# Kernel optimization log

Measured on AMD Instinct MI355X. Metric: run time of the kernel, lower is better.

## Reference

```python
import jax, jax.numpy as jnp
import numpy as np

# dims: B batch, T frames, N tokens/frame, C embed, H heads, D=C//H, MEM memory slots
B, T, N, C = 8, 16, 196, 768
H = 8
D = C // H
MEM = 196          # mem_size; with N=196 -> _init_t = 1, M stays == MEM
HID = 4 * C        # mlp_ratio * embed_dim
STD = 0.02


def _mlp(x, w1, b1, w2, b2):
    # timm-style Mlp: fc1 -> GELU -> fc2 (dropout = 0)
    return jax.nn.gelu(x @ w1 + b1, approximate=False) @ w2 + b2


def _ln(x, w, b, eps=1e-5):
    mu = jnp.mean(x, axis=-1, keepdims=True)
    var = jnp.var(x, axis=-1, keepdims=True)
    return (x - mu) * jax.lax.rsqrt(var + eps) * w + b


def setup_inputs() -> dict:
    key = jax.random.key(0)
    ks = jax.random.split(key, 10)
    f32 = jnp.float32
    return {
        "cur_fea": jax.random.normal(ks[0], (B, T, N, C), f32),
        "norm1_w": jnp.ones((C,), f32), "norm1_b": jnp.zeros((C,), f32),
        "norm2_w": jnp.ones((C,), f32), "norm2_b": jnp.zeros((C,), f32),
        # c_func: Mlp(2C -> 4C -> C)
        "c_w1": jax.random.normal(ks[1], (2 * C, HID), f32) * STD, "c_b1": jnp.zeros((HID,), f32),
        "c_w2": jax.random.normal(ks[2], (HID, C), f32) * STD, "c_b2": jnp.zeros((C,), f32),
        # m_func: Mlp(C -> 4C -> C)
        "m_w1": jax.random.normal(ks[3], (C, HID), f32) * STD, "m_b1": jnp.zeros((HID,), f32),
        "m_w2": jax.random.normal(ks[4], (HID, C), f32) * STD, "m_b2": jnp.zeros((C,), f32),
        # post_func: Mlp(C -> 4C -> C)
        "p_w1": jax.random.normal(ks[5], (C, HID), f32) * STD, "p_b1": jnp.zeros((HID,), f32),
        "p_w2": jax.random.normal(ks[6], (HID, C), f32) * STD, "p_b2": jnp.zeros((C,), f32),
        # ProjectDotDistance: per-head q(c_global) . k(mem) * scale -> sigmoid
        "q_w": jax.random.normal(ks[7], (C, C), f32) * STD, "q_b": jnp.zeros((C,), f32),
        "k_w": jax.random.normal(ks[8], (C, C), f32) * STD, "k_b": jnp.zeros((C,), f32),
    }


def reference(cur_fea, norm1_w, norm1_b, norm2_w, norm2_b,
              c_w1, c_b1, c_w2, c_b2, m_w1, m_b1, m_w2, m_b2,
              p_w1, p_b1, p_w2, p_b2, q_w, q_b, k_w, k_b):
    x = _ln(cur_fea, norm1_w, norm1_b)                       # [B,T,N,C]
    # T*N > mem_size, _init_t = MEM // N = 1 -> init memory = frame 0 (no grad, torch.no_grad)
    init_mem = jax.lax.stop_gradient(x[:, 0].reshape(B, MEM, C))
    scale = D ** -0.5

    def step(mem, fea):                                      # mem [B,MEM,C], fea [B,N,C]
        ap = jnp.mean(mem, axis=1, keepdims=True)            # [B,1,C]
        cg = _mlp(jnp.concatenate([fea, jnp.broadcast_to(ap, fea.shape)], axis=-1),
                  c_w1, c_b1, c_w2, c_b2)                    # [B,N,C]
        memh = _mlp(mem, m_w1, m_b1, m_w2, m_b2).reshape(B, MEM, H, D).transpose(0, 2, 1, 3)  # [B,H,M,D]
        q = (cg @ q_w + q_b).reshape(B, N, H, D).transpose(0, 2, 1, 3)    # [B,H,N,D]
        k = (mem @ k_w + k_b).reshape(B, MEM, H, D).transpose(0, 2, 1, 3) # [B,H,M,D]
        o = jax.nn.sigmoid(jnp.einsum('bhnd,bhmd->bhnm', q, k) * scale)   # [B,H,N,M]
        cgh = cg.reshape(B, N, H, D).transpose(0, 2, 1, 3)               # [B,H,N,D]
        c = jnp.einsum('bhnm,bhnd->bmhd', o, cgh).reshape(B, MEM, C)
        c = _mlp(c, p_w1, p_b1, p_w2, p_b2)
        # mean_N((1-o) * broadcast(memh)) == mean_N(1-o) * memh (memh indep of N)
        gate = jnp.mean(1.0 - o, axis=2)                     # [B,H,M]
        og = (gate[..., None] * memh).transpose(0, 2, 1, 3).reshape(B, MEM, C)
        new_mem = _ln(c + og, norm2_w, norm2_b)
        return new_mem, None

    fea_seq = x[:, 1:].transpose(1, 0, 2, 3)                 # [T-1,B,N,C]
    final_mem, _ = jax.lax.scan(step, init_mem, fea_seq)
    return final_mem                                         # [B,MEM,C]
```

## Files before the change

kernel.cpp:

```cpp
#include <hip/hip_runtime.h>
#include <hip/hip_bf16.h>
#include <math.h>

constexpr int B_   = 8;
constexpr int T_   = 16;
constexpr int N_   = 196;
constexpr int C_   = 768;
constexpr int H_   = 8;
constexpr int D_   = 96;
constexpr int M_   = 196;
constexpr int HID_ = 3072;
constexpr int ROWS_ = B_ * N_;
constexpr int MP_   = 1664;

typedef __hip_bfloat16 bf16;
typedef __attribute__((ext_vector_type(8))) short bf16x8;
typedef __attribute__((ext_vector_type(4))) float f32x4;

__device__ __forceinline__ float b2f(bf16 x) { return __bfloat162float(x); }
__device__ __forceinline__ short bf2s(bf16 x) { union { bf16 b; short s; } u; u.b = x; return u.s; }
__device__ __forceinline__ float s2f(short x) { union { bf16 b; short s; } u; u.s = x; return __bfloat162float(u.b); }

#define GL2LDS(g, l) __builtin_amdgcn_global_load_lds( \
    (__attribute__((address_space(1))) void*)(g), \
    (__attribute__((address_space(3))) void*)(l), 16, 0, 0)

__device__ __forceinline__ void hard_barrier() {
    asm volatile("" ::: "memory");
    __builtin_amdgcn_s_barrier();
    asm volatile("" ::: "memory");
}


__device__ __forceinline__ float block_reduce_sum256(float v, float* sdata) {
    int tid = threadIdx.x;
    sdata[tid] = v;
    __syncthreads();
    for (int s = 128; s > 0; s >>= 1) {
        if (tid < s) sdata[tid] += sdata[tid + s];
        __syncthreads();
    }
    float r = sdata[0];
    __syncthreads();
    return r;
}

struct TEnt { const float* W; bf16* Wt; int K; int N; int tiles; };
struct TEnts { TEnt e[8]; };

__global__ __launch_bounds__(256) void transpose_all_kernel(TEnts tds)
{
    __shared__ float tile[32][33];
    int local = blockIdx.x;
    int i = 0;
    while (i < 7 && local >= tds.e[i].tiles) { local -= tds.e[i].tiles; ++i; }
    TEnt g = tds.e[i];
    int ntx = g.N / 32;
    int n0 = (local % ntx) * 32, k0 = (local / ntx) * 32;
    int tx = threadIdx.x & 31, ty = threadIdx.x >> 5;
#pragma unroll
    for (int r = 0; r < 32; r += 8)
        tile[ty + r][tx] = g.W[(size_t)(k0 + ty + r) * g.N + n0 + tx];
    __syncthreads();
#pragma unroll
    for (int r = 0; r < 32; r += 8)
        g.Wt[(size_t)(n0 + ty + r) * g.K + k0 + tx] = __float2bfloat16(tile[tx][ty + r]);
}

__global__ __launch_bounds__(256) void cvt_kernel(const float* __restrict__ W,
                                                  bf16* __restrict__ o, int n)
{
    int i = blockIdx.x * 256 + threadIdx.x;
    if (i < n) o[i] = __float2bfloat16(W[i]);
}

__global__ __launch_bounds__(256) void ln_frame_kernel(
    const float* __restrict__ cur, int t,
    const float* __restrict__ w, const float* __restrict__ bia,
    bf16* __restrict__ mem_bf, float* __restrict__ app)
{
    __shared__ float sdata[256];
    int row = blockIdx.x;
    int b = row / N_, n = row % N_;
    const float* src = cur + (((size_t)b * T_ + t) * N_ + n) * C_;
    float x[3];
    float sum = 0.f, sumsq = 0.f;
#pragma unroll
    for (int i = 0; i < 3; i++) {
        int c = threadIdx.x + i * 256;
        x[i] = src[c];
        sum += x[i]; sumsq += x[i] * x[i];
    }
    sum = block_reduce_sum256(sum, sdata);
    sumsq = block_reduce_sum256(sumsq, sdata);
    float mu = sum * (1.0f / C_);
    float var = sumsq * (1.0f / C_) - mu * mu;
    float rs = rsqrtf(var + 1e-5f);
#pragma unroll
    for (int i = 0; i < 3; i++) {
        int c = threadIdx.x + i * 256;
        bf16 hv = __float2bfloat16((x[i] - mu) * rs * w[c] + bia[c]);
        mem_bf[(size_t)row * C_ + c] = hv;
        atomicAdd(&app[(size_t)b * C_ + c], b2f(hv));
    }
}

__global__ __launch_bounds__(256) void build_cat_kernel(
    const float* __restrict__ cur, int t,
    const float* __restrict__ w, const float* __restrict__ bia,
    const float* __restrict__ app, bf16* __restrict__ cat)
{
    __shared__ float sdata[256];
    int row = blockIdx.x;
    int b = row / N_, n = row % N_;
    const float* src = cur + (((size_t)b * T_ + t) * N_ + n) * C_;
    float x[3];
    float sum = 0.f, sumsq = 0.f;
#pragma unroll
    for (int i = 0; i < 3; i++) {
        int c = threadIdx.x + i * 256;
        x[i] = src[c];
        sum += x[i]; sumsq += x[i] * x[i];
    }
    sum = block_reduce_sum256(sum, sdata);
    sumsq = block_reduce_sum256(sumsq, sdata);
    float mu = sum * (1.0f / C_);
    float var = sumsq * (1.0f / C_) - mu * mu;
    float rs = rsqrtf(var + 1e-5f);
    bf16* dstrow = cat + (size_t)row * (2 * C_);
#pragma unroll
    for (int i = 0; i < 3; i++) {
        int c = threadIdx.x + i * 256;
        dstrow[c] = __float2bfloat16((x[i] - mu) * rs * w[c] + bia[c]);
        dstrow[C_ + c] = __float2bfloat16(app[(size_t)b * C_ + c] * (1.0f / M_));
    }
}

struct GemmDesc {
    const bf16* A; const bf16* W; const float* bias; bf16* out;
    int K; int N; int ymax; int gelu;
};
struct GemmDescs { GemmDesc d[4]; };

template <int BN>
__global__ __launch_bounds__(256) void mfma_gemm_multi(GemmDescs ds)
{
    constexpr int BM = 128;
    constexpr int TI = 4;
    constexpr int TJ = (BN / 2) / 16;
    constexpr int ABYTES = BM * 128;
    constexpr int BBYTES = BN * 128;
    constexpr int AR = ABYTES / 4096;
    constexpr int BR = BBYTES / 4096;
    constexpr int NL = AR + BR;
    __shared__ short As[2 * BM * 64];
    __shared__ short Bs[2 * BN * 64];

    GemmDesc g = ds.d[blockIdx.z];
    if ((int)blockIdx.y >= g.ymax) return;

    int tid = threadIdx.x;
    int wid = tid >> 6;
    int lane = tid & 63;
    int quad = lane >> 4, l15 = lane & 15;
    int row0 = blockIdx.x * BM;
    int col0 = blockIdx.y * BN;
    int wm = (wid >> 1) * 64;
    int wn = (wid & 1) * (BN / 2);

    f32x4 acc[TI][TJ] = {};

    const char* Ab = (const char*)g.A;
    const char* Wb = (const char*)g.W;
    const size_t Kb = (size_t)g.K * 2;
    const int base = wid * 1024;

    auto stage = [&](int k0, int sel) {
        char* Ad = (char*)As + sel * ABYTES;
        char* Bd = (char*)Bs + sel * BBYTES;
#pragma unroll
        for (int r = 0; r < AR; r++) {
            int o = r * 4096 + base + lane * 16;
            int row = o >> 7, cs = (o >> 4) & 7;
            int kc = cs ^ (row & 7);
            GL2LDS(Ab + (size_t)(row0 + row) * Kb + (size_t)k0 * 2 + kc * 16, Ad + o);
        }
#pragma unroll
        for (int r = 0; r < BR; r++) {
            int o = r * 4096 + base + lane * 16;
            int row = o >> 7, cs = (o >> 4) & 7;
            int kc = cs ^ (row & 7);
            GL2LDS(Wb + (size_t)(col0 + row) * Kb + (size_t)k0 * 2 + kc * 16, Bd + o);
        }
    };

    const int nk = g.K / 64;
    stage(0, 0);
    for (int ki = 0; ki < nk; ki++) {
        int sel = ki & 1;
        if (ki + 1 < nk) {
            stage((ki + 1) * 64, sel ^ 1);
            asm volatile("s_waitcnt vmcnt(%0)" :: "n"(NL) : "memory");
        } else {
            asm volatile("s_waitcnt vmcnt(0)" ::: "memory");
        }
        hard_barrier();
        const bf16x8* Av = (const bf16x8*)(As + sel * BM * 64);
        const bf16x8* Bv = (const bf16x8*)(Bs + sel * BN * 64);
        bf16x8 af[TI][2], bfr[TJ][2];
#pragma unroll
        for (int i = 0; i < TI; i++) {
            int r = wm + i * 16 + l15;
#pragma unroll
            for (int hh = 0; hh < 2; hh++)
                af[i][hh] = Av[r * 8 + ((hh * 4 + quad) ^ (r & 7))];
        }
#pragma unroll
        for (int j = 0; j < TJ; j++) {
            int r = wn + j * 16 + l15;
#pragma unroll
            for (int hh = 0; hh < 2; hh++)
                bfr[j][hh] = Bv[r * 8 + ((hh * 4 + quad) ^ (r & 7))];
        }
#pragma unroll
        for (int hh = 0; hh < 2; hh++)
#pragma unroll
            for (int i = 0; i < TI; i++)
#pragma unroll
                for (int j = 0; j < TJ; j++)
                    acc[i][j] = __builtin_amdgcn_mfma_f32_16x16x32_bf16(
                        af[i][hh], bfr[j][hh], acc[i][j], 0, 0, 0);
        hard_barrier();
    }

#pragma unroll
    for (int i = 0; i < TI; i++) {
        int gr = row0 + wm + i * 16 + quad * 4;
#pragma unroll
        for (int j = 0; j < TJ; j++) {
            int gc = col0 + wn + j * 16 + l15;
            float bv = g.bias ? g.bias[gc] : 0.0f;
#pragma unroll
            for (int r = 0; r < 4; r++) {
                float v = acc[i][j][r] + bv;
                if (g.gelu) v = 0.5f * v * (1.0f + erff(v * 0.7071067811865475f));
                g.out[(size_t)(gr + r) * g.N + gc] = __float2bfloat16(v);
            }
        }
    }
}

__global__ __launch_bounds__(256) void mfma_gemm_splitk(
    const bf16* __restrict__ A, const bf16* __restrict__ Wt,
    float* __restrict__ part, int K)
{
    constexpr int BM = 128;
    constexpr int BN = 64;
    constexpr int TI = 4;
    constexpr int TJ = 2;
    constexpr int ABYTES = BM * 128, BBYTES = BN * 128;
    constexpr int AR = 4, BR = 2, NL = 6;
    __shared__ short As[2 * BM * 64];
    __shared__ short Bs[2 * BN * 64];

    int tid = threadIdx.x;
    int wid = tid >> 6;
    int lane = tid & 63;
    int quad = lane >> 4, l15 = lane & 15;
    int row0 = blockIdx.x * BM;
    int col0 = blockIdx.y * BN;
    int wm = (wid >> 1) * 64;
    int wn = (wid & 1) * 32;
    int kh = K >> 1;
    int kbeg = blockIdx.z * kh;

    f32x4 acc[TI][TJ] = {};
    const char* Ab = (const char*)A;
    const char* Wb = (const char*)Wt;
    const size_t Kb = (size_t)K * 2;
    const int base = wid * 1024;

    auto stage = [&](int k0, int sel) {
        char* Ad = (char*)As + sel * ABYTES;
        char* Bd = (char*)Bs + sel * BBYTES;
#pragma unroll
        for (int r = 0; r < AR; r++) {
            int o = r * 4096 + base + lane * 16;
            int row = o >> 7, cs = (o >> 4) & 7;
            int kc = cs ^ (row & 7);
            GL2LDS(Ab + (size_t)(row0 + row) * Kb + (size_t)k0 * 2 + kc * 16, Ad + o);
        }
#pragma unroll
        for (int r = 0; r < BR; r++) {
            int o = r * 4096 + base + lane * 16;
            int row = o >> 7, cs = (o >> 4) & 7;
            int kc = cs ^ (row & 7);
            GL2LDS(Wb + (size_t)(col0 + row) * Kb + (size_t)k0 * 2 + kc * 16, Bd + o);
        }
    };

    const int nk = kh / 64;
    stage(kbeg, 0);
    for (int ki = 0; ki < nk; ki++) {
        int sel = ki & 1;
        if (ki + 1 < nk) {
            stage(kbeg + (ki + 1) * 64, sel ^ 1);
            asm volatile("s_waitcnt vmcnt(%0)" :: "n"(NL) : "memory");
        } else {
            asm volatile("s_waitcnt vmcnt(0)" ::: "memory");
        }
        hard_barrier();
        const bf16x8* Av = (const bf16x8*)(As + sel * BM * 64);
        const bf16x8* Bv = (const bf16x8*)(Bs + sel * BN * 64);
        bf16x8 af[TI][2], bfr[TJ][2];
#pragma unroll
        for (int i = 0; i < TI; i++) {
            int r = wm + i * 16 + l15;
#pragma unroll
            for (int hh = 0; hh < 2; hh++)
                af[i][hh] = Av[r * 8 + ((hh * 4 + quad) ^ (r & 7))];
        }
#pragma unroll
        for (int j = 0; j < TJ; j++) {
            int r = wn + j * 16 + l15;
#pragma unroll
            for (int hh = 0; hh < 2; hh++)
                bfr[j][hh] = Bv[r * 8 + ((hh * 4 + quad) ^ (r & 7))];
        }
#pragma unroll
        for (int hh = 0; hh < 2; hh++)
#pragma unroll
            for (int i = 0; i < TI; i++)
#pragma unroll
                for (int j = 0; j < TJ; j++)
                    acc[i][j] = __builtin_amdgcn_mfma_f32_16x16x32_bf16(
                        af[i][hh], bfr[j][hh], acc[i][j], 0, 0, 0);
        hard_barrier();
    }

    float* outp = part + (size_t)blockIdx.z * MP_ * C_;
#pragma unroll
    for (int i = 0; i < TI; i++) {
        int gr = row0 + wm + i * 16 + quad * 4;
#pragma unroll
        for (int j = 0; j < TJ; j++) {
            int gc = col0 + wn + j * 16 + l15;
#pragma unroll
            for (int r = 0; r < 4; r++)
                outp[(size_t)(gr + r) * C_ + gc] = acc[i][j][r];
        }
    }
}

__global__ __launch_bounds__(256) void b2q_kernel(
    const float* __restrict__ c_b2, const float* __restrict__ q_b,
    const bf16* __restrict__ W2q_t, float* __restrict__ b2q)
{
    __shared__ float sdata[256];
    int n = blockIdx.x;
    const bf16* row = W2q_t + (size_t)n * HID_;
    float s = 0.f;
    for (int j = threadIdx.x; j < HID_; j += 256) s += c_b2[j] * b2f(row[j]);
    s = block_reduce_sum256(s, sdata);
    if (threadIdx.x == 0) b2q[n] = s + q_b[n];
}

__global__ __launch_bounds__(512) void attn_mfma_kernel(
    const bf16* __restrict__ q, const bf16* __restrict__ k,
    const bf16* __restrict__ cg, bf16* __restrict__ cbuf,
    float* __restrict__ gate)
{
    constexpr int KS = 104;
    constexpr int PSS = 40;
    __shared__ short Ks[64 * KS];
    __shared__ short Qs[32 * KS];
    __shared__ short CGt[96 * PSS];
    __shared__ short Ph[64 * PSS];
    __shared__ short Pl[64 * PSS];
    __shared__ float gred[8][64];

    const int mt = blockIdx.x, h = blockIdx.y, b = blockIdx.z;
    const int m0 = (mt < 3) ? mt * 64 : (M_ - 64);
    const int tid = threadIdx.x;
    const int w = tid >> 6, lane = tid & 63;
    const int quad = lane >> 4, l15 = lane & 15;
    const int wm = w >> 1;
    const int wh = w & 1;
    const float scale = 0.10206207261596575f;

    const bf16* qp = q  + (size_t)b * N_ * C_ + h * D_;
    const bf16* kp = k  + (size_t)b * M_ * C_ + h * D_;
    const bf16* cp = cg + (size_t)b * N_ * C_ + h * D_;

    for (int idx = tid; idx < 64 * 12; idx += 512) {
        int r = idx / 12, c = idx % 12;
        *(bf16x8*)(Ks + r * KS + c * 8) =
            *(const bf16x8*)(kp + (size_t)(m0 + r) * C_ + c * 8);
    }

    f32x4 acc[3] = {};
    float gacc = 0.f;

    const bf16x8 ZEROV = {0, 0, 0, 0, 0, 0, 0, 0};
    bf16x8 qv = ZEROV, cgv = ZEROV;
    const bool active = tid < 32 * 12;
    const int qrow = tid / 12, qcol = (tid % 12) * 8;
    const int cgn = tid & 31, cgd = (tid >> 5) * 8;

    auto issue = [&](int n0) {
        if (!active) return;
        int nq = n0 + qrow;
        qv = (nq < N_) ? *(const bf16x8*)(qp + (size_t)nq * C_ + qcol) : ZEROV;
        int nc = n0 + cgn;
        cgv = (nc < N_) ? *(const bf16x8*)(cp + (size_t)nc * C_ + cgd) : ZEROV;
    };
    auto stage = [&]() {
        if (!active) return;
        *(bf16x8*)(Qs + qrow * KS + qcol) = qv;
#pragma unroll
        for (int i = 0; i < 8; i++) CGt[(cgd + i) * PSS + cgn] = cgv[i];
    };

    issue(0);
    for (int nt = 0; nt < 7; nt++) {
        stage();
        __syncthreads();
        if (nt < 6) issue((nt + 1) * 32);

        f32x4 s4 = {};
#pragma unroll
        for (int kk = 0; kk < 3; kk++) {
            bf16x8 af = *(const bf16x8*)(Ks + (wm * 16 + l15) * KS + kk * 32 + quad * 8);
            bf16x8 bq = *(const bf16x8*)(Qs + (wh * 16 + l15) * KS + kk * 32 + quad * 8);
            s4 = __builtin_amdgcn_mfma_f32_16x16x32_bf16(af, bq, s4, 0, 0, 0);
        }
        const int nglob = nt * 32 + wh * 16 + l15;
#pragma unroll
        for (int r = 0; r < 4; r++) {
            float p = (nglob < N_) ? 1.f / (1.f + expf(-s4[r] * scale)) : 0.f;
            bf16 hb = __float2bfloat16(p);
            bf16 lb = __float2bfloat16(p - __bfloat162float(hb));
            int po = (wm * 16 + quad * 4 + r) * PSS + wh * 16 + l15;
            Ph[po] = bf2s(hb);
            Pl[po] = bf2s(lb);
        }
        __syncthreads();

        {
            const short* ph = Ph + lane * PSS + w * 4;
            const short* pl = Pl + lane * PSS + w * 4;
#pragma unroll
            for (int u = 0; u < 4; u++) gacc += s2f(ph[u]) + s2f(pl[u]);
        }
        bf16x8 pa = *(const bf16x8*)(Ph + (wm * 16 + l15) * PSS + quad * 8);
        bf16x8 pb = *(const bf16x8*)(Pl + (wm * 16 + l15) * PSS + quad * 8);
#pragma unroll
        for (int dt = 0; dt < 3; dt++) {
            bf16x8 bcg = *(const bf16x8*)(CGt + (wh * 48 + dt * 16 + l15) * PSS + quad * 8);
            acc[dt] = __builtin_amdgcn_mfma_f32_16x16x32_bf16(pa, bcg, acc[dt], 0, 0, 0);
            acc[dt] = __builtin_amdgcn_mfma_f32_16x16x32_bf16(pb, bcg, acc[dt], 0, 0, 0);
        }
        __syncthreads();
    }

#pragma unroll
    for (int dt = 0; dt < 3; dt++)
#pragma unroll
        for (int r = 0; r < 4; r++) {
            int m = m0 + wm * 16 + quad * 4 + r;
            cbuf[((size_t)b * M_ + m) * C_ + h * D_ + wh * 48 + dt * 16 + l15] =
                __float2bfloat16(acc[dt][r]);
        }
    gred[w][lane] = gacc;
    __syncthreads();
    if (tid < 64) {
        float g = 0.f;
#pragma unroll
        for (int s = 0; s < 8; s++) g += gred[s][tid];
        gate[((size_t)b * H_ + h) * M_ + m0 + tid] = 1.f - g * (1.0f / N_);
    }
}

__global__ __launch_bounds__(256) void final_kernel(
    const float* __restrict__ part, const float* __restrict__ p_b2,
    const float* __restrict__ gate, const bf16* __restrict__ memh,
    const float* __restrict__ w, const float* __restrict__ bia,
    bf16* __restrict__ mem_bf, float* __restrict__ app, float* __restrict__ outp)
{
    __shared__ float sdata[256];
    int row = blockIdx.x;
    int b = row / M_, m = row % M_;
    float x[3];
    float sum = 0.f, sumsq = 0.f;
#pragma unroll
    for (int i = 0; i < 3; i++) {
        int c = threadIdx.x + i * 256;
        int h = c / D_;
        float v = part[(size_t)row * C_ + c] + part[(size_t)MP_ * C_ + (size_t)row * C_ + c]
                + p_b2[c]
                + gate[(b * H_ + h) * M_ + m] * b2f(memh[(size_t)row * C_ + c]);
        x[i] = v;
        sum += v; sumsq += v * v;
    }
    sum = block_reduce_sum256(sum, sdata);
    sumsq = block_reduce_sum256(sumsq, sdata);
    float mu = sum * (1.0f / C_);
    float var = sumsq * (1.0f / C_) - mu * mu;
    float rs = rsqrtf(var + 1e-5f);
#pragma unroll
    for (int i = 0; i < 3; i++) {
        int c = threadIdx.x + i * 256;
        float v = (x[i] - mu) * rs * w[c] + bia[c];
        bf16 hv = __float2bfloat16(v);
        mem_bf[(size_t)row * C_ + c] = hv;
        atomicAdd(&app[(size_t)b * C_ + c], b2f(hv));
        if (outp) outp[(size_t)row * C_ + c] = v;
    }
}

extern "C" void kernel_launch(void* const* d_in, const int* in_sizes, int n_in,
                              void* d_out, int out_size, void* d_ws, size_t ws_size,
                              hipStream_t stream)
{
    const float* cur_fea = (const float*)d_in[0];
    const float* n1w = (const float*)d_in[1];
    const float* n1b = (const float*)d_in[2];
    const float* n2w = (const float*)d_in[3];
    const float* n2b = (const float*)d_in[4];
    const float* c_w1 = (const float*)d_in[5];
    const float* c_b1 = (const float*)d_in[6];
    const float* c_w2 = (const float*)d_in[7];
    const float* c_b2 = (const float*)d_in[8];
    const float* m_w1 = (const float*)d_in[9];
    const float* m_b1 = (const float*)d_in[10];
    const float* m_w2 = (const float*)d_in[11];
    const float* m_b2 = (const float*)d_in[12];
    const float* p_w1 = (const float*)d_in[13];
    const float* p_b1 = (const float*)d_in[14];
    const float* p_w2 = (const float*)d_in[15];
    const float* p_b2 = (const float*)d_in[16];
    const float* q_w = (const float*)d_in[17];
    const float* q_b = (const float*)d_in[18];
    const float* k_w = (const float*)d_in[19];
    const float* k_b = (const float*)d_in[20];

    size_t off = 0;
    char* base = (char*)d_ws;
    auto carve = [&](size_t bytes) -> char* {
        char* r = base + off;
        off += (bytes + 255) & ~(size_t)255;
        return r;
    };
    bf16* cw1t = (bf16*)carve((size_t)HID_ * (2 * C_) * 2);
    bf16* cw2t = (bf16*)carve((size_t)C_ * HID_ * 2);
    bf16* mw1t = (bf16*)carve((size_t)HID_ * C_ * 2);
    bf16* mw2t = (bf16*)carve((size_t)C_ * HID_ * 2);
    bf16* pw1t = (bf16*)carve((size_t)HID_ * C_ * 2);
    bf16* pw2t = (bf16*)carve((size_t)C_ * HID_ * 2);
    bf16* qwt  = (bf16*)carve((size_t)C_ * C_ * 2);
    bf16* kwt  = (bf16*)carve((size_t)C_ * C_ * 2);
    bf16* mem_bf = (bf16*)carve((size_t)MP_ * C_ * 2);
    char* catreg = carve((size_t)MP_ * 2 * C_ * 2);
    bf16* cat = (bf16*)catreg;
    bf16* qb  = (bf16*)catreg;
    bf16* kb  = (bf16*)catreg + (size_t)MP_ * C_;
    bf16* hid_c = (bf16*)carve((size_t)MP_ * HID_ * 2);
    char* hidm_reg = carve((size_t)MP_ * HID_ * 2);
    bf16*  hid_m = (bf16*)hidm_reg;
    float* part  = (float*)hidm_reg;
    bf16* cg    = (bf16*)carve((size_t)MP_ * C_ * 2);
    bf16* cbuf  = (bf16*)carve((size_t)MP_ * C_ * 2);
    bf16* memh  = (bf16*)carve((size_t)MP_ * C_ * 2);
    float* app  = (float*)carve((size_t)B_ * C_ * 4);
    float* gateb = (float*)carve((size_t)B_ * H_ * M_ * 4);
    float* b2qb  = (float*)carve((size_t)C_ * 4);
    bf16* W2q_t = (bf16*)carve((size_t)C_ * HID_ * 2);
    const bool fuse_q = (off <= ws_size);
    bf16* kb2  = (bf16*)carve((size_t)MP_ * C_ * 2);
    const bool fuse_k = (off <= ws_size);

    const dim3 blk(256);

    {
        TEnts tds;
        tds.e[0] = { c_w1, cw1t, 2 * C_, HID_, (HID_ / 32) * ((2 * C_) / 32) };
        tds.e[1] = { c_w2, cw2t, HID_, C_, (C_ / 32) * (HID_ / 32) };
        tds.e[2] = { m_w1, mw1t, C_, HID_, (HID_ / 32) * (C_ / 32) };
        tds.e[3] = { m_w2, mw2t, HID_, C_, (C_ / 32) * (HID_ / 32) };
        tds.e[4] = { p_w1, pw1t, C_, HID_, (HID_ / 32) * (C_ / 32) };
        tds.e[5] = { p_w2, pw2t, HID_, C_, (C_ / 32) * (HID_ / 32) };
        tds.e[6] = { q_w, qwt, C_, C_, (C_ / 32) * (C_ / 32) };
        tds.e[7] = { k_w, kwt, C_, C_, (C_ / 32) * (C_ / 32) };
        int total = 4608 + 2304 * 5 + 576 * 2;
        transpose_all_kernel<<<total, blk, 0, stream>>>(tds);
    }

    if (fuse_q) {
        bf16* cw2nt = hid_c;
        cvt_kernel<<<(HID_ * C_ + 255) / 256, blk, 0, stream>>>(c_w2, cw2nt, HID_ * C_);
        GemmDescs ds;
        ds.d[0] = { qwt, cw2nt, nullptr, W2q_t, C_, HID_, HID_ / 128, 0 };
        ds.d[1] = ds.d[0]; ds.d[2] = ds.d[0]; ds.d[3] = ds.d[0];
        mfma_gemm_multi<128><<<dim3(C_ / 128, HID_ / 128, 1), blk, 0, stream>>>(ds);
        b2q_kernel<<<C_, blk, 0, stream>>>(c_b2, q_b, W2q_t, b2qb);
    }

    hipMemsetAsync(app, 0, (size_t)B_ * C_ * 4, stream);
    ln_frame_kernel<<<ROWS_, blk, 0, stream>>>(cur_fea, 0, n1w, n1b, mem_bf, app);

    for (int t = 1; t < T_; t++) {
        build_cat_kernel<<<ROWS_, blk, 0, stream>>>(cur_fea, t, n1w, n1b, app, cat);
        hipMemsetAsync(app, 0, (size_t)B_ * C_ * 4, stream);

        {
            GemmDescs ds;
            ds.d[0] = { cat,    cw1t, c_b1, hid_c, 2 * C_, HID_, HID_ / 128, 1 };
            ds.d[1] = { mem_bf, mw1t, m_b1, hid_m, C_,     HID_, HID_ / 128, 1 };
            ds.d[2] = { mem_bf, kwt,  k_b,  kb2,   C_,     C_,   C_ / 128,   0 };
            ds.d[3] = ds.d[0];
            mfma_gemm_multi<128><<<dim3(MP_ / 128, HID_ / 128, fuse_k ? 3 : 2),
                                   blk, 0, stream>>>(ds);
        }
        {
            GemmDescs ds;
            int z = 0;
            ds.d[z++] = { hid_c,  cw2t, c_b2, cg,   HID_, C_, C_ / 64, 0 };
            ds.d[z++] = { hid_m,  mw2t, m_b2, memh, HID_, C_, C_ / 64, 0 };
            if (!fuse_k) ds.d[z++] = { mem_bf, kwt, k_b, kb, C_, C_, C_ / 64, 0 };
            if (fuse_q)  ds.d[z++] = { hid_c, W2q_t, b2qb, qb, HID_, C_, C_ / 64, 0 };
            for (int f = z; f < 4; f++) ds.d[f] = ds.d[0];
            mfma_gemm_multi<64><<<dim3(MP_ / 128, C_ / 64, z), blk, 0, stream>>>(ds);
        }
        if (!fuse_q) {
            GemmDescs ds;
            ds.d[0] = { cg, qwt, q_b, qb, C_, C_, C_ / 64, 0 };
            ds.d[1] = ds.d[0]; ds.d[2] = ds.d[0]; ds.d[3] = ds.d[0];
            mfma_gemm_multi<64><<<dim3(MP_ / 128, C_ / 64, 1), blk, 0, stream>>>(ds);
        }
        attn_mfma_kernel<<<dim3(4, H_, B_), dim3(512), 0, stream>>>(
            qb, fuse_k ? kb2 : kb, cg, cbuf, gateb);
        {
            GemmDescs ds;
            ds.d[0] = { cbuf, pw1t, p_b1, hid_c, C_, HID_, HID_ / 64, 1 };
            ds.d[1] = ds.d[0]; ds.d[2] = ds.d[0]; ds.d[3] = ds.d[0];
            mfma_gemm_multi<64><<<dim3(MP_ / 128, HID_ / 64, 1), blk, 0, stream>>>(ds);
        }
        mfma_gemm_splitk<<<dim3(MP_ / 128, C_ / 64, 2), blk, 0, stream>>>(hid_c, pw2t, part, HID_);
        final_kernel<<<ROWS_, blk, 0, stream>>>(part, p_b2, gateb, memh, n2w, n2b,
                                                mem_bf, app,
                                                (t == T_ - 1) ? (float*)d_out : nullptr);
    }
}
```

Before: 2.793 ms.

## Precompute LayerNorm for all frames once and gather the appended mean inside the GEMM

Runs LayerNorm for frames 1..T-1 in one batched kernel before the scan and stores bf16 results, so the per-step build_cat kernel is removed. The first c_func GEMM now reads its upper half of K from a small per-batch bf16 mean vector through a split-K source pointer, instead of a materialized concatenated matrix. A tiny kernel converts the accumulated mean and resets it, which also replaces a memset. This cuts per-step launches and memory traffic, in exchange for a large extra workspace buffer and a branch in the GEMM staging path.

```diff
diff --git a/kernel.cpp b/kernel.cpp
--- a/kernel.cpp
+++ b/kernel.cpp
@@ -105,6 +105,45 @@
     }
 }
 
+__global__ __launch_bounds__(256) void ln_all_kernel(
+    const float* __restrict__ cur,
+    const float* __restrict__ w, const float* __restrict__ bia,
+    bf16* __restrict__ xln_all)
+{
+    __shared__ float sdata[256];
+    int row = blockIdx.x;
+    int t = blockIdx.y + 1;
+    int b = row / N_, n = row % N_;
+    const float* src = cur + (((size_t)b * T_ + t) * N_ + n) * C_;
+    float x[3];
+    float sum = 0.f, sumsq = 0.f;
+#pragma unroll
+    for (int i = 0; i < 3; i++) {
+        int c = threadIdx.x + i * 256;
+        x[i] = src[c];
+        sum += x[i]; sumsq += x[i] * x[i];
+    }
+    sum = block_reduce_sum256(sum, sdata);
+    sumsq = block_reduce_sum256(sumsq, sdata);
+    float mu = sum * (1.0f / C_);
+    float var = sumsq * (1.0f / C_) - mu * mu;
+    float rs = rsqrtf(var + 1e-5f);
+    bf16* dst = xln_all + ((size_t)(t - 1) * MP_ + row) * C_;
+#pragma unroll
+    for (int i = 0; i < 3; i++) {
+        int c = threadIdx.x + i * 256;
+        dst[c] = __float2bfloat16((x[i] - mu) * rs * w[c] + bia[c]);
+    }
+}
+
+__global__ __launch_bounds__(768) void cvt_app_kernel(float* __restrict__ app,
+                                                      bf16* __restrict__ apbf)
+{
+    size_t i = (size_t)blockIdx.x * C_ + threadIdx.x;
+    apbf[i] = __float2bfloat16(app[i] * (1.0f / M_));
+    app[i] = 0.f;
+}
+
 __global__ __launch_bounds__(256) void build_cat_kernel(
     const float* __restrict__ cur, int t,
     const float* __restrict__ w, const float* __restrict__ bia,
@@ -139,6 +178,7 @@
 struct GemmDesc {
     const bf16* A; const bf16* W; const float* bias; bf16* out;
     int K; int N; int ymax; int gelu;
+    const bf16* A2; int ksplit; int astride;
 };
 struct GemmDescs { GemmDesc d[4]; };
 
@@ -171,19 +211,30 @@
     f32x4 acc[TI][TJ] = {};
 
     const char* Ab = (const char*)g.A;
+    const char* A2b = (const char*)g.A2;
     const char* Wb = (const char*)g.W;
     const size_t Kb = (size_t)g.K * 2;
+    const size_t Asb = (size_t)(g.astride ? g.astride : g.K) * 2;
+    const int ksplit = g.ksplit;
     const int base = wid * 1024;
 
     auto stage = [&](int k0, int sel) {
         char* Ad = (char*)As + sel * ABYTES;
         char* Bd = (char*)Bs + sel * BBYTES;
+        const bool hi = (ksplit != 0) && (k0 >= ksplit);
 #pragma unroll
         for (int r = 0; r < AR; r++) {
             int o = r * 4096 + base + lane * 16;
             int row = o >> 7, cs = (o >> 4) & 7;
             int kc = cs ^ (row & 7);
-            GL2LDS(Ab + (size_t)(row0 + row) * Kb + (size_t)k0 * 2 + kc * 16, Ad + o);
+            const char* src;
+            if (hi) {
+                int bb = (row0 + row) / 196; if (bb > 7) bb = 7;
+                src = A2b + ((size_t)bb * 768 + (k0 - ksplit)) * 2 + kc * 16;
+            } else {
+                src = Ab + (size_t)(row0 + row) * Asb + (size_t)k0 * 2 + kc * 16;
+            }
+            GL2LDS(src, Ad + o);
         }
 #pragma unroll
         for (int r = 0; r < BR; r++) {
@@ -578,6 +629,9 @@
     const bool fuse_q = (off <= ws_size);
     bf16* kb2  = (bf16*)carve((size_t)MP_ * C_ * 2);
     const bool fuse_k = (off <= ws_size);
+    bf16* xln_all = (bf16*)carve((size_t)(T_ - 1) * MP_ * C_ * 2);
+    bf16* apbf    = (bf16*)carve((size_t)B_ * C_ * 2);
+    const bool use_xln = (off <= ws_size);
 
     const dim3 blk(256);
 
@@ -605,18 +659,32 @@
         b2q_kernel<<<C_, blk, 0, stream>>>(c_b2, q_b, W2q_t, b2qb);
     }
 
+    if (use_xln)
+        ln_all_kernel<<<dim3(ROWS_, T_ - 1), blk, 0, stream>>>(cur_fea, n1w, n1b, xln_all);
+
     hipMemsetAsync(app, 0, (size_t)B_ * C_ * 4, stream);
     ln_frame_kernel<<<ROWS_, blk, 0, stream>>>(cur_fea, 0, n1w, n1b, mem_bf, app);
 
     for (int t = 1; t < T_; t++) {
-        build_cat_kernel<<<ROWS_, blk, 0, stream>>>(cur_fea, t, n1w, n1b, app, cat);
-        hipMemsetAsync(app, 0, (size_t)B_ * C_ * 4, stream);
+        const bf16* c1A;
+        if (use_xln) {
+            cvt_app_kernel<<<B_, 768, 0, stream>>>(app, apbf);
+            c1A = xln_all + (size_t)(t - 1) * MP_ * C_;
+        } else {
+            build_cat_kernel<<<ROWS_, blk, 0, stream>>>(cur_fea, t, n1w, n1b, app, cat);
+            hipMemsetAsync(app, 0, (size_t)B_ * C_ * 4, stream);
+            c1A = cat;
+        }
 
         {
             GemmDescs ds;
-            ds.d[0] = { cat,    cw1t, c_b1, hid_c, 2 * C_, HID_, HID_ / 128, 1 };
-            ds.d[1] = { mem_bf, mw1t, m_b1, hid_m, C_,     HID_, HID_ / 128, 1 };
-            ds.d[2] = { mem_bf, kwt,  k_b,  kb2,   C_,     C_,   C_ / 128,   0 };
+            if (use_xln)
+                ds.d[0] = { c1A, cw1t, c_b1, hid_c, 2 * C_, HID_, HID_ / 128, 1,
+                            apbf, C_, C_ };
+            else
+                ds.d[0] = { c1A, cw1t, c_b1, hid_c, 2 * C_, HID_, HID_ / 128, 1 };
+            ds.d[1] = { mem_bf, mw1t, m_b1, hid_m, C_, HID_, HID_ / 128, 1 };
+            ds.d[2] = { mem_bf, kwt,  k_b,  kb2,   C_, C_,   C_ / 128,   0 };
             ds.d[3] = ds.d[0];
             mfma_gemm_multi<128><<<dim3(MP_ / 128, HID_ / 128, fuse_k ? 3 : 2),
                                    blk, 0, stream>>>(ds);
```

Measured after the change: 2.829 ms. Within noise of the previous version (+1.3%).
